# Kernel tuning notes

Hardware: AMD Instinct MI355X
Metric: run time of the kernel (lower is better)

## Reference

```python
import jax, jax.numpy as jnp
import numpy as np

TPS = (10.0, 20.0, 30.0)   # Tps init arg (per-segment period)
EPS = 1e-4                 # jitter added to GP predictive covariance
SEG_LEN = 50               # len(ts[j]) for every segment


def setup_inputs() -> dict:
    key = jax.random.key(0)
    k1, k2, k3 = jax.random.split(key, 3)
    K, M, D, T = 16, 128, 16, 302  # T = 2 + 50 + 100 + 150
    z = jax.random.normal(k1, (K, M, D, T), dtype=jnp.float32)
    # sorted time points in (0, Tp_j) per segment, shape [C, SEG_LEN]
    ts = jnp.sort(jax.random.uniform(k2, (3, SEG_LEN), dtype=jnp.float32)
                  * jnp.asarray(TPS, jnp.float32)[:, None], axis=1)
    # log_tau param (D,), tau around tau_init=1.5
    log_tau = jnp.log(1.0 + jax.random.uniform(k3, (16,), dtype=jnp.float32))
    sldj = jnp.zeros((), jnp.float32)
    return {"z": z, "ts": ts, "log_tau": log_tau, "sum_log_det_jacobians": sldj}


def reference(z, ts, log_tau, sum_log_det_jacobians):
    # z: [K,M,D,T]; ts: [C,SEG_LEN]; log_tau: [D]
    tau = jnp.exp(log_tau)                      # [D]
    z_first = z[..., 0:1]                       # [K,M,D,1]
    z_last = z[..., 1:2]                        # [K,M,D,1]
    z_EP = jnp.concatenate([z_first, z_last], axis=-1)  # [K,M,D,2]
    C, seg = ts.shape
    ts_flat = ts.reshape(-1)
    ldj = sum_log_det_jacobians
    t_ind = 2
    outs = []
    for j in range(C):  # C=3 structurally distinct segment sizes
        m = (j + 1) * seg                       # middle_len
        ts_mid = ts_flat[:m]
        ts_j = jnp.concatenate([jnp.array([0.0, TPS[j]], ts.dtype), ts_mid])  # [m+2]
        ds = ts_j[:, None] - ts_j[None, :]      # [m+2,m+2]
        # squared-exp kernel, batched over all D dims at once
        Kmat = jnp.exp(-(ds ** 2)[None] / (2.0 * tau[:, None, None] ** 2))  # [D,n,n]
        K_EPEP_inv = jnp.linalg.inv(Kmat[:, :2, :2])          # [D,2,2]
        K_predEP = Kmat[:, 2:, :2]                            # [D,m,2]
        A_mu = jnp.einsum('dpe,def->dpf', K_predEP, K_EPEP_inv)  # [D,m,2]
        # conditional mean: A_mu @ z_EP  -> [K,M,D,m]
        z_GP_mu = jnp.einsum('dpe,bsde->bsdp', A_mu, z_EP)
        # conditional covariance  K_predpred - K_predEP K_EPEP^{-1} K_EPpred
        Sigma = Kmat[:, 2:, 2:] - jnp.einsum('dpe,dqe->dpq', A_mu, K_predEP)
        Sigma = Sigma + EPS * jnp.eye(m, dtype=Sigma.dtype)
        L = jnp.linalg.cholesky(Sigma)                        # [D,m,m]
        diag = jnp.diagonal(L, axis1=1, axis2=2)              # [D,m]
        # sum_i log|prod(diag_i)| == sum log|diag| (Cholesky diag > 0)
        ldj = ldj + jnp.sum(jnp.log(jnp.abs(diag)))
        z_mid = z[..., t_ind:t_ind + m]                       # [K,M,D,m]
        t_ind += m
        Lz = jnp.einsum('dpq,bsdq->bsdp', L, z_mid)           # [K,M,D,m]
        z_hat = z_GP_mu + Lz
        outs.append(jnp.concatenate([z_first, z_hat, z_last], axis=-1))  # [K,M,D,m+2]
    z_out = jnp.concatenate(outs, axis=-1)  # [K,M,D, sum_j(m_j+2)] = [16,128,16,306]
    return z_out, ldj
```

## Files before the change

### kernel.cpp

```cpp
#include <hip/hip_runtime.h>

#define LB0_OFF 0
#define LB1_OFF 36864
#define LB2_OFF 158720
#define PART_OFF 373760

typedef __attribute__((ext_vector_type(8))) short bf8_t;
typedef __attribute__((ext_vector_type(8))) unsigned short us8_t;
typedef __attribute__((ext_vector_type(4))) float f32x4;

__device__ __forceinline__ int tri_i(int p) { return (p * (p + 1)) >> 1; }

__device__ __forceinline__ void tri_decode(int e, int& r, int& c) {
  r = (int)((sqrtf(8.0f * (float)e + 1.0f) - 1.0f) * 0.5f);
  if (tri_i(r + 1) <= e) ++r;
  if (tri_i(r) > e) --r;
  c = e - tri_i(r);
}

__device__ __forceinline__ unsigned short f2bf(float f) {
  unsigned u = __builtin_bit_cast(unsigned, f);
  u = (u + 0x7FFFu + ((u >> 16) & 1u)) >> 16;
  return (unsigned short)u;
}

__device__ __forceinline__ float blane(float v, int l) {
  return __builtin_bit_cast(float, __builtin_amdgcn_readlane(__builtin_bit_cast(int, v), l));
}
__device__ __forceinline__ float fastrcp(float x) { return __builtin_amdgcn_rcpf(x); }

#define BNT 512

__global__ __launch_bounds__(BNT) void build_kernel(const float* __restrict__ ts,
                                                    const float* __restrict__ log_tau,
                                                    float* __restrict__ ws)
{
  __shared__ float sS[12880];
  __shared__ __attribute__((aligned(16))) float sU[160 * 20];
  __shared__ __attribute__((aligned(16))) float sW[160 * 20];
  __shared__ float stj[152];
  __shared__ float sAmu[304];
  __shared__ float sKp[304];
  __shared__ float red[8];

  const int j = blockIdx.x >> 4;
  const int d = blockIdx.x & 15;
  const int m = (j + 1) * 50;
  const int mp    = (j == 0) ? 64      : ((j == 1) ? 112     : 160);
  const int ks    = (j == 0) ? 72      : ((j == 1) ? 136     : 168);
  const int lboff = (j == 0) ? LB0_OFF : ((j == 1) ? LB1_OFF : LB2_OFF);
  const float tpsj = (j == 0) ? 10.0f : ((j == 1) ? 20.0f : 30.0f);
  const int tid  = threadIdx.x;
  const int lane = tid & 63;
  const int wid  = tid >> 6;

  const float tau = expf(log_tau[d]);
  const float cc = 1.0f / (2.0f * tau * tau);

  for (int i = tid; i < m; i += BNT) stj[i] = ts[i];
  __syncthreads();

  const float k01 = expf(-tpsj * tpsj * cc);
  const float det = 1.0f - k01 * k01;
  const float i00 = 1.0f / det;
  const float i01 = -k01 / det;

  for (int p = tid; p < m; p += BNT) {
    float tp = stj[p];
    float kp0 = expf(-tp * tp * cc);
    float dt = tp - tpsj;
    float kp1 = expf(-dt * dt * cc);
    sKp[p * 2 + 0] = kp0; sKp[p * 2 + 1] = kp1;
    sAmu[p * 2 + 0] = fmaf(kp0, i00, kp1 * i01);
    sAmu[p * 2 + 1] = fmaf(kp0, i01, kp1 * i00);
  }
  __syncthreads();

  const int tot = tri_i(mp);
  for (int e = tid; e < tot; e += BNT) {
    int r, q;
    tri_decode(e, r, q);
    float v;
    if (r < m) {
      float dq = stj[r] - stj[q];
      v = expf(-dq * dq * cc)
        - fmaf(sAmu[r * 2], sKp[q * 2], sAmu[r * 2 + 1] * sKp[q * 2 + 1]);
      if (r == q) v += 1e-4f;
    } else {
      v = (r == q) ? 1.0f : 0.0f;
    }
    sS[e] = v;
  }
  __syncthreads();

  const int npan = mp >> 4;
  const int tr = lane & 15;
  for (int pb = 0; pb < npan; ++pb) {
    const int kb = pb << 4;
    const int be = kb + 16;
    const int rbase = tri_i(kb + tr) + kb;

    float rd[16];
    float invd[16];
    if (wid < 3) {
#pragma unroll
      for (int q = 0; q < 16; ++q) rd[q] = sS[rbase + q];
#pragma unroll
      for (int kk = 0; kk < 15; ++kk) {
        const float dkk = blane(rd[kk], kk);
        const float ri = fastrcp(dkk);
        invd[kk] = ri;
        const float c = -rd[kk] * ri;
#pragma unroll
        for (int q2 = kk + 1; q2 < 16; ++q2) {
          const float cq2 = blane(rd[kk], q2);
          if (tr > kk && q2 <= tr) rd[q2] = fmaf(c, cq2, rd[q2]);
        }
      }
      invd[15] = fastrcp(blane(rd[15], 15));
    }

    if (be < mp) {
      const int i = be + tid;
      if (i < mp) {
        const int base = tri_i(i) + kb;
        float r[16];
#pragma unroll
        for (int t = 0; t < 16; ++t) r[t] = sS[base + t];
#pragma unroll
        for (int kk = 0; kk < 15; ++kk) {
          const float c = r[kk] * invd[kk];
#pragma unroll
          for (int q = kk + 1; q < 16; ++q)
            r[q] = fmaf(-c, blane(rd[kk], q), r[q]);
        }
#pragma unroll
        for (int t = 0; t < 16; ++t) sS[base + t] = r[t];
        float w[16];
#pragma unroll
        for (int t = 0; t < 16; ++t) w[t] = r[t] * invd[t];
        float4* up = (float4*)&sU[i * 20];
        float4* wp = (float4*)&sW[i * 20];
#pragma unroll
        for (int c4 = 0; c4 < 4; ++c4) {
          up[c4] = *(float4*)&r[c4 * 4];
          wp[c4] = *(float4*)&w[c4 * 4];
        }
      }
    }
    __syncthreads();

    if (wid == 0 && lane < 16) {
#pragma unroll
      for (int q = 0; q < 16; ++q) if (q <= tr) sS[rbase + q] = rd[q];
    }

    if (be < mp) {
      for (int i0 = be + 4 * wid; i0 < mp; i0 += 32) {
        float wreg[4][16];
        int rb[4];
#pragma unroll
        for (int r = 0; r < 4; ++r) {
          const float4* wp = (const float4*)&sW[(i0 + r) * 20];
#pragma unroll
          for (int c4 = 0; c4 < 4; ++c4)
            *(float4*)&wreg[r][c4 * 4] = wp[c4];
          rb[r] = tri_i(i0 + r);
        }
        for (int q0 = be; q0 <= i0 + 3; q0 += 64) {
          const int q = q0 + lane;
          const int qc = (q <= i0 + 3) ? q : (i0 + 3);
          const float4* up = (const float4*)&sU[qc * 20];
          float u[16];
#pragma unroll
          for (int c4 = 0; c4 < 4; ++c4) *(float4*)&u[c4 * 4] = up[c4];
#pragma unroll
          for (int r = 0; r < 4; ++r) {
            if (q <= i0 + r) {
              const int a = rb[r] + q;
              float acc = sS[a];
#pragma unroll
              for (int t = 0; t < 16; ++t) acc = fmaf(-wreg[r][t], u[t], acc);
              sS[a] = acc;
            }
          }
        }
      }
    }
    __syncthreads();
  }

  float part = 0.0f;
  for (int p = tid; p < m; p += BNT) part += 0.5f * logf(sS[tri_i(p) + p]);
#pragma unroll
  for (int off = 32; off > 0; off >>= 1) part += __shfl_down(part, off);
  if (lane == 0) red[wid] = part;
  __syncthreads();
  if (tid == 0) {
    float s = 0.0f;
#pragma unroll
    for (int w8 = 0; w8 < 8; ++w8) s += red[w8];
    ws[PART_OFF + blockIdx.x] = s;
  }

  unsigned* LBg = (unsigned*)ws + lboff + d * (mp * (ks >> 1));
  const int nwords = mp * (ks >> 1);
  for (int idx = tid; idx < nwords; idx += BNT) {
    const int p = idx / (ks >> 1);
    const int k0 = (idx - p * (ks >> 1)) * 2;
    unsigned short h[2];
#pragma unroll
    for (int e = 0; e < 2; ++e) {
      const int k = k0 + e;
      float v = 0.0f;
      if (p < m) {
        if (k < m) {
          if (k <= p) {
            const float dq = sS[tri_i(k) + k];
            v = (k == p) ? sqrtf(dq) : sS[tri_i(p) + k] * rsqrtf(dq);
          }
        } else if (k == m)     v = sAmu[p * 2 + 0];
        else if (k == m + 1)   v = sAmu[p * 2 + 1];
      }
      h[e] = f2bf(v);
    }
    LBg[idx] = (unsigned)h[0] | ((unsigned)h[1] << 16);
  }
}

template <int M, int MP, int KS, int KT, int TOFF, int OOFF, int LBOFF>
__device__ __forceinline__ void apply_impl(const float* __restrict__ z,
                                           const unsigned* __restrict__ wsu,
                                           float* __restrict__ out,
                                           char* smem, int blk)
{
  constexpr int PT = MP / 16;
  constexpr int PTH = (PT + 1) / 2;
  constexpr int CK = KS / 8;
  const int d   = blk & 15;
  const int bs0 = ((blk >> 4) & 63) * 32;
  const int tid = threadIdx.x;
  const int lane = tid & 63;
  const int wv   = tid >> 6;
  const int rt   = wv & 1;
  const int ph   = wv >> 1;

  unsigned short* Zs = (unsigned short*)smem;

  for (int idx = tid; idx < 32 * CK; idx += 256) {
    const int r = idx / CK;
    const int k0 = (idx - r * CK) * 8;
    const float* zr = z + (size_t)((bs0 + r) * 16 + d) * 302;
    us8_t v;
    if (k0 + 8 <= M) {
#pragma unroll
      for (int t = 0; t < 4; ++t) {
        const float2 f = *(const float2*)(zr + TOFF + k0 + 2 * t);
        v[2 * t]     = f2bf(f.x);
        v[2 * t + 1] = f2bf(f.y);
      }
    } else {
#pragma unroll
      for (int e = 0; e < 8; ++e) {
        const int k = k0 + e;
        float f;
        if (k < M)           f = zr[TOFF + k];
        else if (k == M)     f = zr[0];
        else if (k == M + 1) f = zr[1];
        else                 f = 0.0f;
        v[e] = f2bf(f);
      }
    }
    *(us8_t*)&Zs[r * KS + k0] = v;
  }

  if (tid < 64) {
    const int r = tid >> 1;
    const int which = tid & 1;
    const float* zr = z + (size_t)((bs0 + r) * 16 + d) * 302;
    out[(size_t)((bs0 + r) * 16 + d) * 306 + OOFF + (which ? (M + 1) : 0)] = zr[which];
  }
  __syncthreads();

  bf8_t afr[KT];
  {
    const int row = rt * 16 + (lane & 15);
    const int koff = (lane >> 4) * 8;
#pragma unroll
    for (int kt = 0; kt < KT; ++kt)
      afr[kt] = *(const bf8_t*)&Zs[row * KS + kt * 32 + koff];
  }

  const unsigned short* LBd = (const unsigned short*)(wsu + LBOFF + d * (MP * (KS / 2)));
  const int pt0 = ph * PTH;
  const int pt1 = (ph == 0) ? PTH : PT;
  for (int pt = pt0; pt < pt1; ++pt) {
    const int p = pt * 16 + (lane & 15);
    const unsigned short* bb = &LBd[p * KS + (lane >> 4) * 8];
    f32x4 acc = {0.0f, 0.0f, 0.0f, 0.0f};
#pragma unroll
    for (int kt = 0; kt < KT; ++kt) {
      const bf8_t bfr = *(const bf8_t*)&bb[kt * 32];
      acc = __builtin_amdgcn_mfma_f32_16x16x32_bf16(afr[kt], bfr, acc, 0, 0, 0);
    }
    if (p < M) {
      const int rbase = bs0 + rt * 16 + (lane >> 4) * 4;
#pragma unroll
      for (int e = 0; e < 4; ++e)
        out[(size_t)((rbase + e) * 16 + d) * 306 + OOFF + 1 + p] = acc[e];
    }
  }
}

__global__ __launch_bounds__(256) void apply_kernel(const float* __restrict__ z,
                                                    const unsigned* __restrict__ wsu,
                                                    float* __restrict__ out)
{
  __shared__ __attribute__((aligned(16))) char smem[10752];
  const int bid = blockIdx.x;
  if (bid < 1024)      apply_impl<150, 160, 168, 5, 152, 154, LB2_OFF>(z, wsu, out, smem, bid);
  else if (bid < 2048) apply_impl<100, 112, 136, 4,  52,  52, LB1_OFF>(z, wsu, out, smem, bid - 1024);
  else                 apply_impl< 50,  64,  72, 2,   2,   0, LB0_OFF>(z, wsu, out, smem, bid - 2048);
}

__global__ void finalize_kernel(const float* __restrict__ ws_part,
                                const float* __restrict__ sldj,
                                float* __restrict__ out, int last)
{
  if (threadIdx.x == 0) {
    float s = sldj[0];
    for (int i = 0; i < 48; ++i) s += ws_part[i];
    out[last] = s;
  }
}

extern "C" void kernel_launch(void* const* d_in, const int* in_sizes, int n_in,
                              void* d_out, int out_size, void* d_ws, size_t ws_size,
                              hipStream_t stream)
{
  const float* z       = (const float*)d_in[0];
  const float* ts      = (const float*)d_in[1];
  const float* log_tau = (const float*)d_in[2];
  const float* sldj    = (const float*)d_in[3];
  float* out = (float*)d_out;
  float* ws  = (float*)d_ws;

  hipLaunchKernelGGL(build_kernel, dim3(48), dim3(BNT), 0, stream, ts, log_tau, ws);
  hipLaunchKernelGGL(apply_kernel, dim3(3072), dim3(256), 0, stream,
                     z, (const unsigned*)ws, out);
  hipLaunchKernelGGL(finalize_kernel, dim3(1), dim3(64), 0, stream,
                     ws + PART_OFF, sldj, out, out_size - 1);
}
```

Measured before the change: 177.5 us.

## Pipeline blocked Cholesky with lookahead: overlap trailing update with next panel factorization

After: 187.2 us. 1.05x slower.

```diff
diff --git a/kernel.cpp b/kernel.cpp
--- a/kernel.cpp
+++ b/kernel.cpp
@@ -36,8 +36,8 @@
                                                     float* __restrict__ ws)
 {
   __shared__ float sS[12880];
-  __shared__ __attribute__((aligned(16))) float sU[160 * 20];
-  __shared__ __attribute__((aligned(16))) float sW[160 * 20];
+  __shared__ __attribute__((aligned(16))) float sU[2][160 * 20];
+  __shared__ __attribute__((aligned(16))) float sW[2][160 * 20];
   __shared__ float stj[152];
   __shared__ float sAmu[304];
   __shared__ float sKp[304];
@@ -99,12 +99,33 @@
     const int kb = pb << 4;
     const int be = kb + 16;
     const int rbase = tri_i(kb + tr) + kb;
+    float* __restrict__ sUp = sU[pb & 1];
+    float* __restrict__ sWp = sW[pb & 1];
+    const float* __restrict__ sUq = sU[(pb & 1) ^ 1];
+    const float* __restrict__ sWq = sW[(pb & 1) ^ 1];
 
     float rd[16];
     float invd[16];
     if (wid < 3) {
 #pragma unroll
       for (int q = 0; q < 16; ++q) rd[q] = sS[rbase + q];
+      if (pb > 0) {
+        float wp[16];
+        const float4* wv = (const float4*)&sWq[(kb + tr) * 20];
+#pragma unroll
+        for (int c4 = 0; c4 < 4; ++c4) *(float4*)&wp[c4 * 4] = wv[c4];
+#pragma unroll
+        for (int q = 0; q < 16; ++q) {
+          const float4* uv = (const float4*)&sUq[(kb + q) * 20];
+          float u[16];
+#pragma unroll
+          for (int c4 = 0; c4 < 4; ++c4) *(float4*)&u[c4 * 4] = uv[c4];
+          float acc = 0.0f;
+#pragma unroll
+          for (int s = 0; s < 16; ++s) acc = fmaf(wp[s], u[s], acc);
+          rd[q] -= acc;
+        }
+      }
 #pragma unroll
       for (int kk = 0; kk < 15; ++kk) {
         const float dkk = blane(rd[kk], kk);
@@ -118,50 +139,68 @@
         }
       }
       invd[15] = fastrcp(blane(rd[15], 15));
-    }
-
-    if (be < mp) {
-      const int i = be + tid;
-      if (i < mp) {
-        const int base = tri_i(i) + kb;
-        float r[16];
-#pragma unroll
-        for (int t = 0; t < 16; ++t) r[t] = sS[base + t];
-#pragma unroll
-        for (int kk = 0; kk < 15; ++kk) {
-          const float c = r[kk] * invd[kk];
-#pragma unroll
-          for (int q = kk + 1; q < 16; ++q)
-            r[q] = fmaf(-c, blane(rd[kk], q), r[q]);
-        }
-#pragma unroll
-        for (int t = 0; t < 16; ++t) sS[base + t] = r[t];
-        float w[16];
-#pragma unroll
-        for (int t = 0; t < 16; ++t) w[t] = r[t] * invd[t];
-        float4* up = (float4*)&sU[i * 20];
-        float4* wp = (float4*)&sW[i * 20];
+    } else if (pb > 0) {
+      const int nel = (mp - be) * 16;
+      for (int e = tid - 192; e < nel; e += 320) {
+        const int row = be + (e >> 4);
+        const int col = kb + (e & 15);
+        float wr[16], ur[16];
+        const float4* wv = (const float4*)&sWq[row * 20];
+        const float4* uv = (const float4*)&sUq[col * 20];
 #pragma unroll
         for (int c4 = 0; c4 < 4; ++c4) {
-          up[c4] = *(float4*)&r[c4 * 4];
-          wp[c4] = *(float4*)&w[c4 * 4];
-        }
+          *(float4*)&wr[c4 * 4] = wv[c4];
+          *(float4*)&ur[c4 * 4] = uv[c4];
+        }
+        const int a = tri_i(row) + col;
+        float acc = sS[a];
+#pragma unroll
+        for (int s = 0; s < 16; ++s) acc = fmaf(-wr[s], ur[s], acc);
+        sS[a] = acc;
       }
     }
     __syncthreads();
 
-    if (wid == 0 && lane < 16) {
-#pragma unroll
-      for (int q = 0; q < 16; ++q) if (q <= tr) sS[rbase + q] = rd[q];
-    }
-
-    if (be < mp) {
-      for (int i0 = be + 4 * wid; i0 < mp; i0 += 32) {
+    if (wid < 3) {
+      if (be < mp) {
+        const int i = be + tid;
+        if (i < mp) {
+          const int base = tri_i(i) + kb;
+          float r[16];
+#pragma unroll
+          for (int t = 0; t < 16; ++t) r[t] = sS[base + t];
+#pragma unroll
+          for (int kk = 0; kk < 15; ++kk) {
+            const float c = r[kk] * invd[kk];
+#pragma unroll
+            for (int q = kk + 1; q < 16; ++q)
+              r[q] = fmaf(-c, blane(rd[kk], q), r[q]);
+          }
+#pragma unroll
+          for (int t = 0; t < 16; ++t) sS[base + t] = r[t];
+          float w[16];
+#pragma unroll
+          for (int t = 0; t < 16; ++t) w[t] = r[t] * invd[t];
+          float4* up = (float4*)&sUp[i * 20];
+          float4* wp = (float4*)&sWp[i * 20];
+#pragma unroll
+          for (int c4 = 0; c4 < 4; ++c4) {
+            up[c4] = *(float4*)&r[c4 * 4];
+            wp[c4] = *(float4*)&w[c4 * 4];
+          }
+        }
+      }
+      if (wid == 0 && lane < 16) {
+#pragma unroll
+        for (int q = 0; q < 16; ++q) if (q <= tr) sS[rbase + q] = rd[q];
+      }
+    } else if (pb > 0) {
+      for (int i0 = be + 4 * (wid - 3); i0 < mp; i0 += 20) {
         float wreg[4][16];
         int rb[4];
 #pragma unroll
         for (int r = 0; r < 4; ++r) {
-          const float4* wp = (const float4*)&sW[(i0 + r) * 20];
+          const float4* wp = (const float4*)&sWq[(i0 + r) * 20];
 #pragma unroll
           for (int c4 = 0; c4 < 4; ++c4)
             *(float4*)&wreg[r][c4 * 4] = wp[c4];
@@ -170,7 +209,7 @@
         for (int q0 = be; q0 <= i0 + 3; q0 += 64) {
           const int q = q0 + lane;
           const int qc = (q <= i0 + 3) ? q : (i0 + 3);
-          const float4* up = (const float4*)&sU[qc * 20];
+          const float4* up = (const float4*)&sUq[qc * 20];
           float u[16];
 #pragma unroll
           for (int c4 = 0; c4 < 4; ++c4) *(float4*)&u[c4 * 4] = up[c4];
```

## Template build kernel per segment, pad packed rows, fold finalize into apply

Applied to the files above, without the earlier changes.

After: 176.0 us. About the same (-0.8%).

```diff
diff --git a/kernel.cpp b/kernel.cpp
--- a/kernel.cpp
+++ b/kernel.cpp
@@ -10,6 +10,11 @@
 typedef __attribute__((ext_vector_type(4))) float f32x4;
 
 __device__ __forceinline__ int tri_i(int p) { return (p * (p + 1)) >> 1; }
+
+__device__ __forceinline__ int roff(int p) {
+  const int T = p >> 2, r = p & 3;
+  return ((T + 1) * (2 * T + r)) << 2;
+}
 
 __device__ __forceinline__ void tri_decode(int e, int& r, int& c) {
   r = (int)((sqrtf(8.0f * (float)e + 1.0f) - 1.0f) * 0.5f);
@@ -31,11 +36,209 @@
 
 #define BNT 512
 
+template <int J>
+__device__ __forceinline__ void build_impl(int d,
+                                           const float* __restrict__ ts,
+                                           const float* __restrict__ log_tau,
+                                           float* __restrict__ ws,
+                                           float* sS, float* sU, float* sW,
+                                           float* stj, float* sAmu, float* sKp,
+                                           float* red)
+{
+  constexpr int M  = (J + 1) * 50;
+  constexpr int MP = (J == 0) ? 64 : ((J == 1) ? 112 : 160);
+  constexpr int KS = (J == 0) ? 72 : ((J == 1) ? 136 : 168);
+  constexpr int LBOFF = (J == 0) ? LB0_OFF : ((J == 1) ? LB1_OFF : LB2_OFF);
+  constexpr float TPSJ = (J == 0) ? 10.0f : ((J == 1) ? 20.0f : 30.0f);
+  constexpr int KW = KS / 2;
+  constexpr int TOT = (MP * (MP + 1)) / 2;
+  constexpr int NPAN = MP / 16;
+
+  const int tid  = threadIdx.x;
+  const int lane = tid & 63;
+  const int wid  = tid >> 6;
+
+  const float tau = expf(log_tau[d]);
+  const float cc = 1.0f / (2.0f * tau * tau);
+
+  for (int i = tid; i < M; i += BNT) stj[i] = ts[i];
+  __syncthreads();
+
+  const float k01 = expf(-TPSJ * TPSJ * cc);
+  const float det = 1.0f - k01 * k01;
+  const float i00 = 1.0f / det;
+  const float i01 = -k01 / det;
+
+  for (int p = tid; p < M; p += BNT) {
+    float tp = stj[p];
+    float kp0 = expf(-tp * tp * cc);
+    float dt = tp - TPSJ;
+    float kp1 = expf(-dt * dt * cc);
+    sKp[p * 2 + 0] = kp0; sKp[p * 2 + 1] = kp1;
+    sAmu[p * 2 + 0] = fmaf(kp0, i00, kp1 * i01);
+    sAmu[p * 2 + 1] = fmaf(kp0, i01, kp1 * i00);
+  }
+  __syncthreads();
+
+  for (int e = tid; e < TOT; e += BNT) {
+    int r, q;
+    tri_decode(e, r, q);
+    float v;
+    if (r < M) {
+      float dq = stj[r] - stj[q];
+      v = expf(-dq * dq * cc)
+        - fmaf(sAmu[r * 2], sKp[q * 2], sAmu[r * 2 + 1] * sKp[q * 2 + 1]);
+      if (r == q) v += 1e-4f;
+    } else {
+      v = (r == q) ? 1.0f : 0.0f;
+    }
+    sS[roff(r) + q] = v;
+  }
+  __syncthreads();
+
+  const int tr = lane & 15;
+#pragma unroll 1
+  for (int pb = 0; pb < NPAN; ++pb) {
+    const int kb = pb << 4;
+    const int be = kb + 16;
+    const int rbase = roff(kb + tr) + kb;
+
+    float rd[16];
+    float invd[16];
+    if (wid < 3) {
+      const float4* rp = (const float4*)&sS[rbase];
+#pragma unroll
+      for (int c4 = 0; c4 < 4; ++c4) *(float4*)&rd[c4 * 4] = rp[c4];
+#pragma unroll
+      for (int kk = 0; kk < 15; ++kk) {
+        const float dkk = blane(rd[kk], kk);
+        const float ri = fastrcp(dkk);
+        invd[kk] = ri;
+        const float c = -rd[kk] * ri;
+#pragma unroll
+        for (int q2 = kk + 1; q2 < 16; ++q2) {
+          const float cq2 = blane(rd[kk], q2);
+          if (tr > kk && q2 <= tr) rd[q2] = fmaf(c, cq2, rd[q2]);
+        }
+      }
+      invd[15] = fastrcp(blane(rd[15], 15));
+    }
+
+    if (be < MP) {
+      const int i = be + tid;
+      if (i < MP) {
+        const int base = roff(i) + kb;
+        float r[16];
+        const float4* rp = (const float4*)&sS[base];
+#pragma unroll
+        for (int c4 = 0; c4 < 4; ++c4) *(float4*)&r[c4 * 4] = rp[c4];
+#pragma unroll
+        for (int kk = 0; kk < 15; ++kk) {
+          const float c = r[kk] * invd[kk];
+#pragma unroll
+          for (int q = kk + 1; q < 16; ++q)
+            r[q] = fmaf(-c, blane(rd[kk], q), r[q]);
+        }
+        float4* sp = (float4*)&sS[base];
+#pragma unroll
+        for (int c4 = 0; c4 < 4; ++c4) sp[c4] = *(float4*)&r[c4 * 4];
+        float w[16];
+#pragma unroll
+        for (int t = 0; t < 16; ++t) w[t] = r[t] * invd[t];
+        float4* up = (float4*)&sU[i * 20];
+        float4* wp = (float4*)&sW[i * 20];
+#pragma unroll
+        for (int c4 = 0; c4 < 4; ++c4) {
+          up[c4] = *(float4*)&r[c4 * 4];
+          wp[c4] = *(float4*)&w[c4 * 4];
+        }
+      }
+    }
+    __syncthreads();
+
+    if (wid == 0 && lane < 16) {
+#pragma unroll
+      for (int q = 0; q < 16; ++q) if (q <= tr) sS[rbase + q] = rd[q];
+    }
+
+    if (be < MP) {
+      for (int i0 = be + 4 * wid; i0 < MP; i0 += 32) {
+        float wreg[4][16];
+        int rb[4];
+#pragma unroll
+        for (int r = 0; r < 4; ++r) {
+          const float4* wp = (const float4*)&sW[(i0 + r) * 20];
+#pragma unroll
+          for (int c4 = 0; c4 < 4; ++c4)
+            *(float4*)&wreg[r][c4 * 4] = wp[c4];
+          rb[r] = roff(i0 + r);
+        }
+        for (int q0 = be; q0 <= i0 + 3; q0 += 64) {
+          const int q = q0 + lane;
+          const int qc = (q <= i0 + 3) ? q : (i0 + 3);
+          const float4* up = (const float4*)&sU[qc * 20];
+          float u[16];
+#pragma unroll
+          for (int c4 = 0; c4 < 4; ++c4) *(float4*)&u[c4 * 4] = up[c4];
+#pragma unroll
+          for (int r = 0; r < 4; ++r) {
+            if (q <= i0 + r) {
+              const int a = rb[r] + q;
+              float acc = sS[a];
+#pragma unroll
+              for (int t = 0; t < 16; ++t) acc = fmaf(-wreg[r][t], u[t], acc);
+              sS[a] = acc;
+            }
+          }
+        }
+      }
+    }
+    __syncthreads();
+  }
+
+  float part = 0.0f;
+  for (int p = tid; p < M; p += BNT) part += 0.5f * logf(sS[roff(p) + p]);
+#pragma unroll
+  for (int off = 32; off > 0; off >>= 1) part += __shfl_down(part, off);
+  if (lane == 0) red[wid] = part;
+  __syncthreads();
+  if (tid == 0) {
+    float s = 0.0f;
+#pragma unroll
+    for (int w8 = 0; w8 < 8; ++w8) s += red[w8];
+    ws[PART_OFF + J * 16 + d] = s;
+  }
+
+  unsigned* LBg = (unsigned*)ws + LBOFF + d * (MP * KW);
+  constexpr int NWORDS = MP * KW;
+  for (int idx = tid; idx < NWORDS; idx += BNT) {
+    const int p = idx / KW;
+    const int k0 = (idx - p * KW) * 2;
+    unsigned short h[2];
+#pragma unroll
+    for (int e = 0; e < 2; ++e) {
+      const int k = k0 + e;
+      float v = 0.0f;
+      if (p < M) {
+        if (k < M) {
+          if (k <= p) {
+            const float dq = sS[roff(k) + k];
+            v = (k == p) ? sqrtf(dq) : sS[roff(p) + k] * rsqrtf(dq);
+          }
+        } else if (k == M)     v = sAmu[p * 2 + 0];
+        else if (k == M + 1)   v = sAmu[p * 2 + 1];
+      }
+      h[e] = f2bf(v);
+    }
+    LBg[idx] = (unsigned)h[0] | ((unsigned)h[1] << 16);
+  }
+}
+
 __global__ __launch_bounds__(BNT) void build_kernel(const float* __restrict__ ts,
                                                     const float* __restrict__ log_tau,
                                                     float* __restrict__ ws)
 {
-  __shared__ float sS[12880];
+  __shared__ float sS[13120];
   __shared__ __attribute__((aligned(16))) float sU[160 * 20];
   __shared__ __attribute__((aligned(16))) float sW[160 * 20];
   __shared__ float stj[152];
@@ -45,187 +248,9 @@
 
   const int j = blockIdx.x >> 4;
   const int d = blockIdx.x & 15;
-  const int m = (j + 1) * 50;
-  const int mp    = (j == 0) ? 64      : ((j == 1) ? 112     : 160);
-  const int ks    = (j == 0) ? 72      : ((j == 1) ? 136     : 168);
-  const int lboff = (j == 0) ? LB0_OFF : ((j == 1) ? LB1_OFF : LB2_OFF);
-  const float tpsj = (j == 0) ? 10.0f : ((j == 1) ? 20.0f : 30.0f);
-  const int tid  = threadIdx.x;
-  const int lane = tid & 63;
-  const int wid  = tid >> 6;
-
-  const float tau = expf(log_tau[d]);
-  const float cc = 1.0f / (2.0f * tau * tau);
-
-  for (int i = tid; i < m; i += BNT) stj[i] = ts[i];
-  __syncthreads();
-
-  const float k01 = expf(-tpsj * tpsj * cc);
-  const float det = 1.0f - k01 * k01;
-  const float i00 = 1.0f / det;
-  const float i01 = -k01 / det;
-
-  for (int p = tid; p < m; p += BNT) {
-    float tp = stj[p];
-    float kp0 = expf(-tp * tp * cc);
-    float dt = tp - tpsj;
-    float kp1 = expf(-dt * dt * cc);
-    sKp[p * 2 + 0] = kp0; sKp[p * 2 + 1] = kp1;
-    sAmu[p * 2 + 0] = fmaf(kp0, i00, kp1 * i01);
-    sAmu[p * 2 + 1] = fmaf(kp0, i01, kp1 * i00);
-  }
-  __syncthreads();
-
-  const int tot = tri_i(mp);
-  for (int e = tid; e < tot; e += BNT) {
-    int r, q;
-    tri_decode(e, r, q);
-    float v;
-    if (r < m) {
-      float dq = stj[r] - stj[q];
-      v = expf(-dq * dq * cc)
-        - fmaf(sAmu[r * 2], sKp[q * 2], sAmu[r * 2 + 1] * sKp[q * 2 + 1]);
-      if (r == q) v += 1e-4f;
-    } else {
-      v = (r == q) ? 1.0f : 0.0f;
-    }
-    sS[e] = v;
-  }
-  __syncthreads();
-
-  const int npan = mp >> 4;
-  const int tr = lane & 15;
-  for (int pb = 0; pb < npan; ++pb) {
-    const int kb = pb << 4;
-    const int be = kb + 16;
-    const int rbase = tri_i(kb + tr) + kb;
-
-    float rd[16];
-    float invd[16];
-    if (wid < 3) {
-#pragma unroll
-      for (int q = 0; q < 16; ++q) rd[q] = sS[rbase + q];
-#pragma unroll
-      for (int kk = 0; kk < 15; ++kk) {
-        const float dkk = blane(rd[kk], kk);
-        const float ri = fastrcp(dkk);
-        invd[kk] = ri;
-        const float c = -rd[kk] * ri;
-#pragma unroll
-        for (int q2 = kk + 1; q2 < 16; ++q2) {
-          const float cq2 = blane(rd[kk], q2);
-          if (tr > kk && q2 <= tr) rd[q2] = fmaf(c, cq2, rd[q2]);
-        }
-      }
-      invd[15] = fastrcp(blane(rd[15], 15));
-    }
-
-    if (be < mp) {
-      const int i = be + tid;
-      if (i < mp) {
-        const int base = tri_i(i) + kb;
-        float r[16];
-#pragma unroll
-        for (int t = 0; t < 16; ++t) r[t] = sS[base + t];
-#pragma unroll
-        for (int kk = 0; kk < 15; ++kk) {
-          const float c = r[kk] * invd[kk];
-#pragma unroll
-          for (int q = kk + 1; q < 16; ++q)
-            r[q] = fmaf(-c, blane(rd[kk], q), r[q]);
-        }
-#pragma unroll
-        for (int t = 0; t < 16; ++t) sS[base + t] = r[t];
-        float w[16];
-#pragma unroll
-        for (int t = 0; t < 16; ++t) w[t] = r[t] * invd[t];
-        float4* up = (float4*)&sU[i * 20];
-        float4* wp = (float4*)&sW[i * 20];
-#pragma unroll
-        for (int c4 = 0; c4 < 4; ++c4) {
-          up[c4] = *(float4*)&r[c4 * 4];
-          wp[c4] = *(float4*)&w[c4 * 4];
-        }
-      }
-    }
-    __syncthreads();
-
-    if (wid == 0 && lane < 16) {
-#pragma unroll
-      for (int q = 0; q < 16; ++q) if (q <= tr) sS[rbase + q] = rd[q];
-    }
-
-    if (be < mp) {
-      for (int i0 = be + 4 * wid; i0 < mp; i0 += 32) {
-        float wreg[4][16];
-        int rb[4];
-#pragma unroll
-        for (int r = 0; r < 4; ++r) {
-          const float4* wp = (const float4*)&sW[(i0 + r) * 20];
-#pragma unroll
-          for (int c4 = 0; c4 < 4; ++c4)
-            *(float4*)&wreg[r][c4 * 4] = wp[c4];
-          rb[r] = tri_i(i0 + r);
-        }
-        for (int q0 = be; q0 <= i0 + 3; q0 += 64) {
-          const int q = q0 + lane;
-          const int qc = (q <= i0 + 3) ? q : (i0 + 3);
-          const float4* up = (const float4*)&sU[qc * 20];
-          float u[16];
-#pragma unroll
-          for (int c4 = 0; c4 < 4; ++c4) *(float4*)&u[c4 * 4] = up[c4];
-#pragma unroll
-          for (int r = 0; r < 4; ++r) {
-            if (q <= i0 + r) {
-              const int a = rb[r] + q;
-              float acc = sS[a];
-#pragma unroll
-              for (int t = 0; t < 16; ++t) acc = fmaf(-wreg[r][t], u[t], acc);
-              sS[a] = acc;
-            }
-          }
-        }
-      }
-    }
-    __syncthreads();
-  }
-
-  float part = 0.0f;
-  for (int p = tid; p < m; p += BNT) part += 0.5f * logf(sS[tri_i(p) + p]);
-#pragma unroll
-  for (int off = 32; off > 0; off >>= 1) part += __shfl_down(part, off);
-  if (lane == 0) red[wid] = part;
-  __syncthreads();
-  if (tid == 0) {
-    float s = 0.0f;
-#pragma unroll
-    for (int w8 = 0; w8 < 8; ++w8) s += red[w8];
-    ws[PART_OFF + blockIdx.x] = s;
-  }
-
-  unsigned* LBg = (unsigned*)ws + lboff + d * (mp * (ks >> 1));
-  const int nwords = mp * (ks >> 1);
-  for (int idx = tid; idx < nwords; idx += BNT) {
-    const int p = idx / (ks >> 1);
-    const int k0 = (idx - p * (ks >> 1)) * 2;
-    unsigned short h[2];
-#pragma unroll
-    for (int e = 0; e < 2; ++e) {
-      const int k = k0 + e;
-      float v = 0.0f;
-      if (p < m) {
-        if (k < m) {
-          if (k <= p) {
-            const float dq = sS[tri_i(k) + k];
-            v = (k == p) ? sqrtf(dq) : sS[tri_i(p) + k] * rsqrtf(dq);
-          }
-        } else if (k == m)     v = sAmu[p * 2 + 0];
-        else if (k == m + 1)   v = sAmu[p * 2 + 1];
-      }
-      h[e] = f2bf(v);
-    }
-    LBg[idx] = (unsigned)h[0] | ((unsigned)h[1] << 16);
-  }
+  if (j == 0)      build_impl<0>(d, ts, log_tau, ws, sS, sU, sW, stj, sAmu, sKp, red);
+  else if (j == 1) build_impl<1>(d, ts, log_tau, ws, sS, sU, sW, stj, sAmu, sKp, red);
+  else             build_impl<2>(d, ts, log_tau, ws, sS, sU, sW, stj, sAmu, sKp, red);
 }
 
 template <int M, int MP, int KS, int KT, int TOFF, int OOFF, int LBOFF>
@@ -314,24 +339,22 @@
 
 __global__ __launch_bounds__(256) void apply_kernel(const float* __restrict__ z,
                                                     const unsigned* __restrict__ wsu,
-                                                    float* __restrict__ out)
+                                                    float* __restrict__ out,
+                                                    const float* __restrict__ part,
+                                                    const float* __restrict__ sldj,
+                                                    int last)
 {
   __shared__ __attribute__((aligned(16))) char smem[10752];
   const int bid = blockIdx.x;
+  if (bid == 3071 && threadIdx.x == 0) {
+    float s = sldj[0];
+#pragma unroll
+    for (int i = 0; i < 48; ++i) s += part[i];
+    out[last] = s;
+  }
   if (bid < 1024)      apply_impl<150, 160, 168, 5, 152, 154, LB2_OFF>(z, wsu, out, smem, bid);
   else if (bid < 2048) apply_impl<100, 112, 136, 4,  52,  52, LB1_OFF>(z, wsu, out, smem, bid - 1024);
   else                 apply_impl< 50,  64,  72, 2,   2,   0, LB0_OFF>(z, wsu, out, smem, bid - 2048);
-}
-
-__global__ void finalize_kernel(const float* __restrict__ ws_part,
-                                const float* __restrict__ sldj,
-                                float* __restrict__ out, int last)
-{
-  if (threadIdx.x == 0) {
-    float s = sldj[0];
-    for (int i = 0; i < 48; ++i) s += ws_part[i];
-    out[last] = s;
-  }
 }
 
 extern "C" void kernel_launch(void* const* d_in, const int* in_sizes, int n_in,
@@ -347,7 +370,6 @@
 
   hipLaunchKernelGGL(build_kernel, dim3(48), dim3(BNT), 0, stream, ts, log_tau, ws);
   hipLaunchKernelGGL(apply_kernel, dim3(3072), dim3(256), 0, stream,
-                     z, (const unsigned*)ws, out);
-  hipLaunchKernelGGL(finalize_kernel, dim3(1), dim3(64), 0, stream,
-                     ws + PART_OFF, sldj, out, out_size - 1);
-}
+                     z, (const unsigned*)ws, out,
+                     ws + PART_OFF, sldj, out_size - 1);
+}
```
